# Kernel optimization log

Hardware: AMD Instinct MI355X
Metric: run time of the kernel (lower is better)

The kernel has to match this reference:

```python
import jax, jax.numpy as jnp
import numpy as np

B, DIM, N = 4, 256, 2048
DIM_CTX, M = 256, 2048
HEADS, DIM_HEAD = 8, 64
DIM_INNER = HEADS * DIM_HEAD  # 512
EPS = 1e-12  # matches F.normalize eps


def setup_inputs() -> dict:
    key = jax.random.key(0)
    ks = jax.random.split(key, 8)
    return {
        "fmap": jax.random.normal(ks[0], (B, DIM, N), dtype=jnp.float32),
        "context": jax.random.normal(ks[1], (B, DIM_CTX, M), dtype=jnp.float32),
        "mask": jax.random.randint(ks[2], (B, M), 0, 2) > 0,
        "gamma": jnp.ones((DIM, 1), dtype=jnp.float32),
        "gamma_ctx": jnp.ones((DIM_CTX, 1), dtype=jnp.float32),
        "Wq": jax.random.normal(ks[3], (DIM_INNER, DIM), dtype=jnp.float32) * (DIM ** -0.5),
        "Wkv": jax.random.normal(ks[4], (2 * DIM_INNER, DIM_CTX), dtype=jnp.float32) * (DIM_CTX ** -0.5),
        "Wout": jax.random.normal(ks[5], (DIM, DIM_INNER), dtype=jnp.float32) * (DIM_INNER ** -0.5),
    }


def channel_rmsnorm(x, gamma):
    # F.normalize(x, dim=1) * sqrt(dim) * gamma ; x: [b, c, n], gamma: [c, 1]
    scale = x.shape[1] ** 0.5
    norm = jnp.sqrt(jnp.sum(x * x, axis=1, keepdims=True))
    normed = x / jnp.maximum(norm, EPS)
    return normed * scale * gamma[None]


def reference(fmap, context, mask, gamma, gamma_ctx, Wq, Wkv, Wout):
    h, d = HEADS, DIM_HEAD
    attn_scale = d ** -0.5

    fmap_n = channel_rmsnorm(fmap, gamma)          # [b, dim, n]
    ctx_n = channel_rmsnorm(context, gamma_ctx)    # [b, dim_ctx, m]

    # 1x1 Conv1d == matmul over channels
    q = jnp.einsum('oc,bcn->bon', Wq, fmap_n)      # [b, h*d, n]
    kv = jnp.einsum('oc,bcm->bom', Wkv, ctx_n)     # [b, 2*h*d, m]
    k, v = jnp.split(kv, 2, axis=1)

    # [b, h*d, n] -> [b, h, n, d]
    def to_heads(t):
        b, _, nn = t.shape
        return t.reshape(b, h, d, nn).transpose(0, 1, 3, 2)

    q, k, v = to_heads(q), to_heads(k), to_heads(v)

    # L2-distance attention: sim = -||q_i - k_j||_2 * scale
    q2 = jnp.sum(q * q, axis=-1)                   # [b, h, n]
    k2 = jnp.sum(k * k, axis=-1)                   # [b, h, m]
    qk = jnp.einsum('bhid,bhjd->bhij', q, k)       # [b, h, n, m]
    d2 = jnp.maximum(q2[..., :, None] + k2[..., None, :] - 2.0 * qk, 0.0)
    dist = jnp.sqrt(jnp.maximum(d2, EPS))
    sim = -dist * attn_scale

    neg_max = -jnp.finfo(sim.dtype).max
    sim = jnp.where(mask[:, None, None, :], sim, neg_max)

    attn = jax.nn.softmax(sim, axis=-1)            # [b, h, n, m]
    out = jnp.einsum('bhij,bhjd->bhid', attn, v)   # [b, h, n, d]
    out = out.transpose(0, 1, 3, 2).reshape(out.shape[0], h * d, -1)  # [b, h*d, n]
    return jnp.einsum('oc,bcn->bon', Wout, out)    # [b, dim, n]
```

## Files before the change

### kernel.cpp

```cpp
#include <hip/hip_runtime.h>
#include <hip/hip_bf16.h>

#define B_ 4
#define DIM_ 256
#define N_ 2048
#define M_ 2048
#define HEADS_ 8
#define DHEAD_ 64
#define DINNER_ 512

typedef __attribute__((ext_vector_type(8))) short short8;
typedef __attribute__((ext_vector_type(4))) short short4v;
typedef __attribute__((ext_vector_type(4))) float floatx4;
typedef __attribute__((ext_vector_type(4))) _Float16 half4;
typedef __attribute__((ext_vector_type(8))) _Float16 half8;

#if defined(__has_builtin)
#if __has_builtin(__builtin_amdgcn_global_load_lds)
#define HAS_DMA 1
#endif
#endif

typedef __attribute__((address_space(1))) const void gvoid_t;
typedef __attribute__((address_space(3))) void lvoid_t;

#define CQ_ 0.18033688011112042f
#define NEG2CQ_ (-0.36067376022224084f)
#define EPS2_ 3.25213893e-14f

__device__ inline short bf16r(float x) {
  unsigned u = __float_as_uint(x);
  unsigned r = (u + 0x7fffu + ((u >> 16) & 1u)) >> 16;
  return (short)r;
}
__device__ inline float bf2f(short b) {
  return __uint_as_float(((unsigned)(unsigned short)b) << 16);
}

__global__ __launch_bounds__(256) void wsplit_kernel(
    const float* __restrict__ Wq, const float* __restrict__ Wkv,
    const float* __restrict__ Wout, const float* __restrict__ gamma,
    const float* __restrict__ gctx, short* __restrict__ whi,
    short* __restrict__ wlo) {
  const int y = blockIdx.y;
  const int gsz[3] = {32768, 65536, 32768};
  const int goff[3] = {0, 131072, 393216};
  int gidx = blockIdx.x * 256 + threadIdx.x;
  if (gidx >= gsz[y]) return;
  const float* W = (y == 0) ? Wq : (y == 1) ? Wkv : Wout;
  const int cmask = (y == 2) ? 511 : 255;
  int e0 = gidx * 4;
  int c = e0 & cmask;
  float4 wv = *(const float4*)&W[e0];
  if (y < 2) {
    const float* g = (y == 0) ? gamma : gctx;
    float4 g4 = *(const float4*)&g[c];
    wv.x *= g4.x; wv.y *= g4.y; wv.z *= g4.z; wv.w *= g4.w;
  }
  float vv[4] = {wv.x, wv.y, wv.z, wv.w};
  short4v hi, lo;
#pragma unroll
  for (int e = 0; e < 4; ++e) {
    short hb = bf16r(vv[e]);
    hi[e] = hb;
    lo[e] = bf16r(vv[e] - bf2f(hb));
  }
  *(short4v*)&whi[goff[y] + e0] = hi;
  *(short4v*)&wlo[goff[y] + e0] = lo;
}

__global__ __launch_bounds__(256) void colnorm_t_kernel(
    const float* __restrict__ xf, const float* __restrict__ xc,
    short* __restrict__ xtf, short* __restrict__ xtc, int NN) {
  const float* x = (blockIdx.z == 0) ? xf : xc;
  short* xt = (blockIdx.z == 0) ? xtf : xtc;
  int b = blockIdx.y;
  int tx = threadIdx.x, ty = threadIdx.y;
  int n0 = blockIdx.x * 64, n = n0 + tx;
  const float* xb = x + (size_t)b * 256 * NN;

  float ssq = 0.f;
  for (int c = ty; c < 256; c += 4) {
    float v = xb[(size_t)c * NN + n];
    ssq += v * v;
  }
  __shared__ float red[4][64];
  __shared__ float scl[64];
  __shared__ float t[64][65];
  red[ty][tx] = ssq;
  __syncthreads();
  if (ty == 0) {
    float s = red[0][tx] + red[1][tx] + red[2][tx] + red[3][tx];
    scl[tx] = 16.0f / fmaxf(sqrtf(s), 1e-12f);
  }
  int tid = ty * 64 + tx;
  int row = tid >> 2, cg = tid & 3;
  for (int c0 = 0; c0 < 256; c0 += 64) {
    __syncthreads();
    for (int cc = ty; cc < 64; cc += 4) t[cc][tx] = xb[(size_t)(c0 + cc) * NN + n];
    __syncthreads();
    float sc = scl[row];
    short8 o0v, o1v;
#pragma unroll
    for (int e = 0; e < 8; ++e) {
      o0v[e] = bf16r(t[cg * 16 + e][row] * sc);
      o1v[e] = bf16r(t[cg * 16 + 8 + e][row] * sc);
    }
    size_t base = ((size_t)b * NN + n0 + row) * 256 + c0 + cg * 16;
    *(short8*)&xt[base] = o0v;
    *(short8*)&xt[base + 8] = o1v;
  }
}

__global__ __launch_bounds__(256) void qkv_gemm_kernel(
    const short* __restrict__ whi, const short* __restrict__ wlo,
    const short* __restrict__ fmap_t, const short* __restrict__ ctx_t,
    short* __restrict__ qb, short* __restrict__ kc, _Float16* __restrict__ vc,
    const int* __restrict__ maskp, float* __restrict__ k2m) {
  const int b = blockIdx.z;
  const int y = blockIdx.y;
  const bool isq = (y < 4);
  const int o0 = (isq ? y : y - 4) * 128;
  const int n0 = blockIdx.x * 128;
  const short* Wh = whi + (isq ? 0 : 131072);
  const short* Wl = wlo + (isq ? 0 : 131072);
  const short* Xt = isq ? fmap_t : ctx_t;

  const int tid = threadIdx.x;
  const int w = tid >> 6, l = tid & 63, quad = l >> 4, l15 = l & 15;
  const int wo = (w >> 1) * 64, wn = (w & 1) * 64;

  __shared__ __align__(16) short Wa[2][128][40];
  __shared__ __align__(16) short Xb[128][40];

  floatx4 acc[4][4];
#pragma unroll
  for (int ot = 0; ot < 4; ++ot)
#pragma unroll
    for (int nt = 0; nt < 4; ++nt)
#pragma unroll
      for (int r = 0; r < 4; ++r) acc[ot][nt][r] = 0.f;

  for (int c0 = 0; c0 < 256; c0 += 32) {
    __syncthreads();
#pragma unroll
    for (int it = 0; it < 2; ++it) {
      int lin = tid + it * 256;
      int row = lin >> 2, sg = (lin & 3) * 8;
      size_t src = (size_t)(o0 + row) * 256 + c0 + sg;
      *(short8*)&Wa[0][row][sg] = *(const short8*)&Wh[src];
      *(short8*)&Wa[1][row][sg] = *(const short8*)&Wl[src];
    }
#pragma unroll
    for (int it = 0; it < 2; ++it) {
      int lin = tid + it * 256;
      int nn = lin >> 2, sg = (lin & 3) * 8;
      *(short8*)&Xb[nn][sg] =
          *(const short8*)&Xt[((size_t)b * 2048 + n0 + nn) * 256 + c0 + sg];
    }
    __syncthreads();

    short8 ah[4], al[4], bx[4];
#pragma unroll
    for (int ot = 0; ot < 4; ++ot) {
      ah[ot] = *(const short8*)&Wa[0][wo + 16 * ot + l15][8 * quad];
      al[ot] = *(const short8*)&Wa[1][wo + 16 * ot + l15][8 * quad];
    }
#pragma unroll
    for (int nt = 0; nt < 4; ++nt)
      bx[nt] = *(const short8*)&Xb[wn + 16 * nt + l15][8 * quad];
#pragma unroll
    for (int ot = 0; ot < 4; ++ot)
#pragma unroll
      for (int nt = 0; nt < 4; ++nt) {
        acc[ot][nt] =
            __builtin_amdgcn_mfma_f32_16x16x32_bf16(al[ot], bx[nt], acc[ot][nt], 0, 0, 0);
        acc[ot][nt] =
            __builtin_amdgcn_mfma_f32_16x16x32_bf16(ah[ot], bx[nt], acc[ot][nt], 0, 0, 0);
      }
  }

  if (isq) {
#pragma unroll
    for (int nt = 0; nt < 4; ++nt) {
      int n = n0 + wn + 16 * nt + l15;
      size_t base = ((size_t)b * 2048 + n) * 512;
#pragma unroll
      for (int ot = 0; ot < 4; ++ot) {
        int o = o0 + wo + 16 * ot + 4 * quad;
        short4v pk;
#pragma unroll
        for (int r = 0; r < 4; ++r) pk[r] = bf16r(CQ_ * acc[ot][nt][r]);
        *(short4v*)&qb[base + o] = pk;
      }
    }
  } else if (o0 < 512) {
    const int head = (o0 + wo) >> 6;
    const int bh = b * 8 + head;
    float k2p[4] = {0.f, 0.f, 0.f, 0.f};
#pragma unroll
    for (int nt = 0; nt < 4; ++nt) {
      int m = n0 + wn + 16 * nt + l15;
      int chunk = m >> 6, mrow = m & 63;
      size_t tbase = (((size_t)bh * 32 + chunk) * 64 + mrow) * 64;
      int sw = mrow & 7;
#pragma unroll
      for (int ot = 0; ot < 4; ++ot) {
        int d0 = 16 * ot + 4 * quad;
        short4v pk;
#pragma unroll
        for (int r = 0; r < 4; ++r) {
          short pv = bf16r(NEG2CQ_ * acc[ot][nt][r]);
          pk[r] = pv;
          float kr = bf2f(pv);
          k2p[nt] += kr * kr;
        }
        *(short4v*)&kc[tbase + (size_t)(((d0 >> 3) ^ sw) << 3) + (d0 & 7)] = pk;
      }
    }
#pragma unroll
    for (int nt = 0; nt < 4; ++nt) {
      float s = k2p[nt];
      s += __shfl_xor(s, 16);
      s += __shfl_xor(s, 32);
      if (quad == 0) {
        int m = n0 + wn + 16 * nt + l15;
        int mv = maskp[b * 2048 + m];
        k2m[(size_t)bh * 2048 + m] = mv ? 0.25f * s : __builtin_inff();
      }
    }
  } else {
    const int chv = o0 - 512 + wo;
    const int bh = b * 8 + (chv >> 6);
#pragma unroll
    for (int nt = 0; nt < 4; ++nt) {
      int j = n0 + wn + 16 * nt + l15;
      int chunk = j >> 6, jr = j & 63;
      int jrem = jr & 31;
      int colp = 32 * (jr >> 5) + ((jrem >> 2) & 3) * 8 + (jrem >> 4) * 4 +
                 (jrem & 3);
      size_t cbase = ((size_t)bh * 32 + chunk) * 4096;
#pragma unroll
      for (int ot = 0; ot < 4; ++ot)
#pragma unroll
        for (int r = 0; r < 4; ++r) {
          int drow = (chv + 16 * ot + 4 * quad + r) & 63;
          vc[cbase + drow * 64 + (((colp >> 3) ^ (drow & 7)) << 3) +
             (colp & 7)] = (_Float16)acc[ot][nt][r];
        }
    }
  }
}

__global__ __launch_bounds__(512, 8) void attn_kernel(
    const short* __restrict__ qb, const short* __restrict__ kc,
    const _Float16* __restrict__ vc, const float* __restrict__ k2m,
    short* __restrict__ attn_t) {
  const int bid = blockIdx.x;
  const int rr = bid & 7, qq = bid >> 3;
  const int bh = rr * 4 + (qq >> 5);
  const int iblk = qq & 31;
  const int h = bh & 7, b = bh >> 3;
  const int i0 = iblk * 64;

  const int tid = threadIdx.x;
  const int w = tid >> 6, l = tid & 63, quad = l >> 4, l15 = l & 15;
  const int wr = w >> 1, jh = w & 1;

  __shared__ __align__(16) short sbuf[2][2][4096];

  const short* qrow =
      qb + ((size_t)b * 2048 + i0 + 16 * wr + l15) * 512 + h * 64;
  const short* kcb = kc + (size_t)bh * 32 * 4096;
  const _Float16* vcb = vc + (size_t)bh * 32 * 4096;
  const float* k2b = k2m + (size_t)bh * 2048;

  short8 qa0 = *(const short8*)&qrow[8 * quad];
  short8 qa1 = *(const short8*)&qrow[32 + 8 * quad];
  float q2p = 0.f;
#pragma unroll
  for (int jj = 0; jj < 8; ++jj) {
    float f0 = bf2f(qa0[jj]), f1 = bf2f(qa1[jj]);
    q2p += f0 * f0 + f1 * f1;
  }
  q2p += __shfl_xor(q2p, 16);
  q2p += __shfl_xor(q2p, 32);
  const float q2c = q2p;

  floatx4 accO[4];
#pragma unroll
  for (int dt = 0; dt < 4; ++dt)
#pragma unroll
    for (int r = 0; r < 4; ++r) accO[dt][r] = 0.f;
  float lsum = 0.f;

  const int sx = l15 & 7;

  auto stage = [&](int c, int p) {
    const short* ks = kcb + (size_t)c * 4096 + w * 512 + l * 8;
    const _Float16* vs = vcb + (size_t)c * 4096 + w * 512 + l * 8;
#ifdef HAS_DMA
    __builtin_amdgcn_global_load_lds((gvoid_t*)ks,
                                     (lvoid_t*)&sbuf[0][p][w * 512], 16, 0, 0);
    __builtin_amdgcn_global_load_lds((gvoid_t*)vs,
                                     (lvoid_t*)&sbuf[1][p][w * 512], 16, 0, 0);
#else
    *(short8*)&sbuf[0][p][w * 512 + l * 8] = *(const short8*)ks;
    *(half8*)&((_Float16*)sbuf[1][p])[w * 512 + l * 8] = *(const half8*)vs;
#endif
  };

  stage(0, 0);
  for (int c = 0; c < 32; ++c) {
    __syncthreads();
    if (c < 31) stage(c + 1, (c + 1) & 1);
    const int p = c & 1;

    half8 pb;
#pragma unroll
    for (int jt = 0; jt < 2; ++jt) {
      float4 k2v = *(const float4*)&k2b[c * 64 + jh * 32 + 16 * jt + 4 * quad];
      const short* kr = &sbuf[0][p][(jh * 32 + 16 * jt + l15) * 64];
      short8 k0 = *(const short8*)&kr[(quad ^ sx) << 3];
      short8 k1 = *(const short8*)&kr[((quad + 4) ^ sx) << 3];
      floatx4 a;
      a[0] = q2c + k2v.x;
      a[1] = q2c + k2v.y;
      a[2] = q2c + k2v.z;
      a[3] = q2c + k2v.w;
      __builtin_amdgcn_s_setprio(1);
      a = __builtin_amdgcn_mfma_f32_16x16x32_bf16(k0, qa0, a, 0, 0, 0);
      a = __builtin_amdgcn_mfma_f32_16x16x32_bf16(k1, qa1, a, 0, 0, 0);
      __builtin_amdgcn_s_setprio(0);
#pragma unroll
      for (int r = 0; r < 4; ++r) {
        float s = __builtin_amdgcn_sqrtf(fmaxf(a[r], EPS2_));
        float pv = __builtin_amdgcn_exp2f(-s);
        lsum += pv;
        pb[4 * jt + r] = (_Float16)pv;
      }
    }

    __builtin_amdgcn_s_setprio(1);
#pragma unroll
    for (int dt = 0; dt < 4; ++dt) {
      const _Float16* vr = (const _Float16*)&sbuf[1][p][(16 * dt + l15) * 64];
      half8 hh = *(const half8*)&vr[((quad + 4 * jh) ^ sx) << 3];
      accO[dt] =
          __builtin_amdgcn_mfma_f32_16x16x32_f16(hh, pb, accO[dt], 0, 0, 0);
    }
    __builtin_amdgcn_s_setprio(0);
  }

  __syncthreads();
  float* scr = (float*)sbuf;
  const int sidx = (wr * 64 + l) * 17;
  if (jh) {
#pragma unroll
    for (int dt = 0; dt < 4; ++dt)
#pragma unroll
      for (int r = 0; r < 4; ++r) scr[sidx + dt * 4 + r] = accO[dt][r];
    scr[sidx + 16] = lsum;
  }
  __syncthreads();
  if (!jh) {
#pragma unroll
    for (int dt = 0; dt < 4; ++dt)
#pragma unroll
      for (int r = 0; r < 4; ++r) accO[dt][r] += scr[sidx + dt * 4 + r];
    lsum += scr[sidx + 16];
    lsum += __shfl_xor(lsum, 16);
    lsum += __shfl_xor(lsum, 32);
    float rl = 1.0f / lsum;
    size_t base = ((size_t)b * 2048 + i0 + 16 * wr + l15) * 512 + h * 64;
#pragma unroll
    for (int dt = 0; dt < 4; ++dt) {
      short4v pk;
#pragma unroll
      for (int r = 0; r < 4; ++r) pk[r] = bf16r(accO[dt][r] * rl);
      *(short4v*)&attn_t[base + 16 * dt + 4 * quad] = pk;
    }
  }
}

__global__ __launch_bounds__(256) void outproj_kernel(
    const short* __restrict__ whi, const short* __restrict__ wlo,
    const short* __restrict__ Xt, float* __restrict__ Yf) {
  const int b = blockIdx.z;
  const int n0 = blockIdx.x * 128;
  const int o0 = blockIdx.y * 64;
  const int tid = threadIdx.x;
  const int w = tid >> 6, l = tid & 63, quad = l >> 4, l15 = l & 15;
  const int wo = (w >> 1) * 32, wn = (w & 1) * 64;

  __shared__ __align__(16) short Wa[2][64][40];
  __shared__ __align__(16) short Xb[128][40];

  floatx4 acc[2][4];
#pragma unroll
  for (int ot = 0; ot < 2; ++ot)
#pragma unroll
    for (int nt = 0; nt < 4; ++nt)
#pragma unroll
      for (int r = 0; r < 4; ++r) acc[ot][nt][r] = 0.f;

  for (int c0 = 0; c0 < 512; c0 += 32) {
    __syncthreads();
    {
      int row = tid >> 2, sg = (tid & 3) * 8;
      size_t src = (size_t)(o0 + row) * 512 + c0 + sg;
      *(short8*)&Wa[0][row][sg] = *(const short8*)&whi[src];
      *(short8*)&Wa[1][row][sg] = *(const short8*)&wlo[src];
    }
#pragma unroll
    for (int it = 0; it < 2; ++it) {
      int lin = tid + it * 256;
      int nn = lin >> 2, sg = (lin & 3) * 8;
      *(short8*)&Xb[nn][sg] =
          *(const short8*)&Xt[((size_t)b * 2048 + n0 + nn) * 512 + c0 + sg];
    }
    __syncthreads();

    short8 ah[2], al[2], bx[4];
#pragma unroll
    for (int ot = 0; ot < 2; ++ot) {
      ah[ot] = *(const short8*)&Wa[0][wo + 16 * ot + l15][8 * quad];
      al[ot] = *(const short8*)&Wa[1][wo + 16 * ot + l15][8 * quad];
    }
#pragma unroll
    for (int nt = 0; nt < 4; ++nt)
      bx[nt] = *(const short8*)&Xb[wn + 16 * nt + l15][8 * quad];
#pragma unroll
    for (int ot = 0; ot < 2; ++ot)
#pragma unroll
      for (int nt = 0; nt < 4; ++nt) {
        acc[ot][nt] =
            __builtin_amdgcn_mfma_f32_16x16x32_bf16(al[ot], bx[nt], acc[ot][nt], 0, 0, 0);
        acc[ot][nt] =
            __builtin_amdgcn_mfma_f32_16x16x32_bf16(ah[ot], bx[nt], acc[ot][nt], 0, 0, 0);
      }
  }

#pragma unroll
  for (int ot = 0; ot < 2; ++ot)
#pragma unroll
    for (int r = 0; r < 4; ++r) {
      int o = o0 + wo + 16 * ot + 4 * quad + r;
#pragma unroll
      for (int nt = 0; nt < 4; ++nt)
        Yf[((size_t)b * 256 + o) * 2048 + n0 + wn + 16 * nt + l15] =
            acc[ot][nt][r];
    }
}

extern "C" void kernel_launch(void* const* d_in, const int* in_sizes, int n_in,
                              void* d_out, int out_size, void* d_ws,
                              size_t ws_size, hipStream_t stream) {
  const float* fmap = (const float*)d_in[0];
  const float* context = (const float*)d_in[1];
  const int* mask = (const int*)d_in[2];
  const float* gamma = (const float*)d_in[3];
  const float* gamma_ctx = (const float*)d_in[4];
  const float* Wq = (const float*)d_in[5];
  const float* Wkv = (const float*)d_in[6];
  const float* Wout = (const float*)d_in[7];
  float* out = (float*)d_out;

  char* ws = (char*)d_ws;
  short* fmap_t = (short*)ws;
  short* ctx_t = fmap_t + 2097152;
  short* qb = ctx_t + 2097152;
  short* kc = qb + 4194304;
  _Float16* vc = (_Float16*)(kc + 4194304);
  short* attn_t = (short*)(vc + 4194304);
  float* k2m = (float*)(attn_t + 4194304);
  short* whi = (short*)(k2m + 65536);
  short* wlo = whi + 524288;

  dim3 blk64x4(64, 4);
  wsplit_kernel<<<dim3(256, 3), 256, 0, stream>>>(Wq, Wkv, Wout, gamma,
                                                  gamma_ctx, whi, wlo);
  colnorm_t_kernel<<<dim3(32, B_, 2), blk64x4, 0, stream>>>(
      fmap, context, fmap_t, ctx_t, N_);
  qkv_gemm_kernel<<<dim3(16, 12, B_), 256, 0, stream>>>(
      whi, wlo, fmap_t, ctx_t, qb, kc, vc, mask, k2m);
  attn_kernel<<<dim3(1024), 512, 0, stream>>>(qb, kc, vc, k2m, attn_t);
  outproj_kernel<<<dim3(16, 4, B_), 256, 0, stream>>>(whi + 393216,
                                                      wlo + 393216, attn_t,
                                                      out);
}
```

Measured before the change: 206.3 us.

## Software-pipeline PV MFMA one chunk behind QK and softmax in attention loop

Restructures the attention main loop so the P·V MFMAs for chunk c-1 are issued while chunk c's QK MFMAs and sqrt/exp2 work are in flight. V staging is delayed by one iteration into its own double buffer, and K gets its own double buffer. A final epilogue applies the last chunk's PV. The aim is to overlap transcendental VALU work with matrix-core work and remove the serial dependency between softmax and PV within an iteration. In exchange, the probabilities must stay live across iterations, which adds register pressure, and V is loaded with less lead time before it is used.

```diff
diff --git a/kernel.cpp b/kernel.cpp
--- a/kernel.cpp
+++ b/kernel.cpp
@@ -267,7 +267,7 @@
   const int w = tid >> 6, l = tid & 63, quad = l >> 4, l15 = l & 15;
   const int wr = w >> 1, jh = w & 1;
 
-  __shared__ __align__(16) short sbuf[2][2][4096];
+  __shared__ __align__(16) short sbuf[4][4096];
 
   const short* qrow =
       qb + ((size_t)b * 2048 + i0 + 16 * wr + l15) * 512 + h * 64;
@@ -296,60 +296,97 @@
 
   const int sx = l15 & 7;
 
-  auto stage = [&](int c, int p) {
+  auto stageK = [&](int c, int p) {
     const short* ks = kcb + (size_t)c * 4096 + w * 512 + l * 8;
+#ifdef HAS_DMA
+    __builtin_amdgcn_global_load_lds((gvoid_t*)ks,
+                                     (lvoid_t*)&sbuf[p][w * 512], 16, 0, 0);
+#else
+    *(short8*)&sbuf[p][w * 512 + l * 8] = *(const short8*)ks;
+#endif
+  };
+  auto stageV = [&](int c, int p) {
     const _Float16* vs = vcb + (size_t)c * 4096 + w * 512 + l * 8;
 #ifdef HAS_DMA
-    __builtin_amdgcn_global_load_lds((gvoid_t*)ks,
-                                     (lvoid_t*)&sbuf[0][p][w * 512], 16, 0, 0);
     __builtin_amdgcn_global_load_lds((gvoid_t*)vs,
-                                     (lvoid_t*)&sbuf[1][p][w * 512], 16, 0, 0);
+                                     (lvoid_t*)&sbuf[2 + p][w * 512], 16, 0, 0);
 #else
-    *(short8*)&sbuf[0][p][w * 512 + l * 8] = *(const short8*)ks;
-    *(half8*)&((_Float16*)sbuf[1][p])[w * 512 + l * 8] = *(const half8*)vs;
+    *(half8*)&((_Float16*)sbuf[2 + p])[w * 512 + l * 8] = *(const half8*)vs;
 #endif
   };
 
-  stage(0, 0);
+  stageK(0, 0);
+  half8 pbprev;
   for (int c = 0; c < 32; ++c) {
     __syncthreads();
-    if (c < 31) stage(c + 1, (c + 1) & 1);
     const int p = c & 1;
-
-    half8 pb;
-#pragma unroll
-    for (int jt = 0; jt < 2; ++jt) {
-      float4 k2v = *(const float4*)&k2b[c * 64 + jh * 32 + 16 * jt + 4 * quad];
-      const short* kr = &sbuf[0][p][(jh * 32 + 16 * jt + l15) * 64];
+    if (c < 31) stageK(c + 1, p ^ 1);
+    stageV(c, p);
+
+    floatx4 a0, a1;
+    {
+      float4 k2v = *(const float4*)&k2b[c * 64 + jh * 32 + 4 * quad];
+      const short* kr = &sbuf[p][(jh * 32 + l15) * 64];
       short8 k0 = *(const short8*)&kr[(quad ^ sx) << 3];
       short8 k1 = *(const short8*)&kr[((quad + 4) ^ sx) << 3];
-      floatx4 a;
-      a[0] = q2c + k2v.x;
-      a[1] = q2c + k2v.y;
-      a[2] = q2c + k2v.z;
-      a[3] = q2c + k2v.w;
+      a0[0] = q2c + k2v.x; a0[1] = q2c + k2v.y;
+      a0[2] = q2c + k2v.z; a0[3] = q2c + k2v.w;
       __builtin_amdgcn_s_setprio(1);
-      a = __builtin_amdgcn_mfma_f32_16x16x32_bf16(k0, qa0, a, 0, 0, 0);
-      a = __builtin_amdgcn_mfma_f32_16x16x32_bf16(k1, qa1, a, 0, 0, 0);
+      a0 = __builtin_amdgcn_mfma_f32_16x16x32_bf16(k0, qa0, a0, 0, 0, 0);
+      a0 = __builtin_amdgcn_mfma_f32_16x16x32_bf16(k1, qa1, a0, 0, 0, 0);
       __builtin_amdgcn_s_setprio(0);
-#pragma unroll
-      for (int r = 0; r < 4; ++r) {
-        float s = __builtin_amdgcn_sqrtf(fmaxf(a[r], EPS2_));
-        float pv = __builtin_amdgcn_exp2f(-s);
-        lsum += pv;
-        pb[4 * jt + r] = (_Float16)pv;
+    }
+    {
+      float4 k2v = *(const float4*)&k2b[c * 64 + jh * 32 + 16 + 4 * quad];
+      const short* kr = &sbuf[p][(jh * 32 + 16 + l15) * 64];
+      short8 k0 = *(const short8*)&kr[(quad ^ sx) << 3];
+      short8 k1 = *(const short8*)&kr[((quad + 4) ^ sx) << 3];
+      a1[0] = q2c + k2v.x; a1[1] = q2c + k2v.y;
+      a1[2] = q2c + k2v.z; a1[3] = q2c + k2v.w;
+      __builtin_amdgcn_s_setprio(1);
+      a1 = __builtin_amdgcn_mfma_f32_16x16x32_bf16(k0, qa0, a1, 0, 0, 0);
+      a1 = __builtin_amdgcn_mfma_f32_16x16x32_bf16(k1, qa1, a1, 0, 0, 0);
+      __builtin_amdgcn_s_setprio(0);
+    }
+
+    if (c > 0) {
+      __builtin_amdgcn_s_setprio(1);
+#pragma unroll
+      for (int dt = 0; dt < 4; ++dt) {
+        const _Float16* vr =
+            (const _Float16*)&sbuf[2 + (p ^ 1)][(16 * dt + l15) * 64];
+        half8 hh = *(const half8*)&vr[((quad + 4 * jh) ^ sx) << 3];
+        accO[dt] =
+            __builtin_amdgcn_mfma_f32_16x16x32_f16(hh, pbprev, accO[dt], 0, 0, 0);
       }
-    }
-
-    __builtin_amdgcn_s_setprio(1);
-#pragma unroll
-    for (int dt = 0; dt < 4; ++dt) {
-      const _Float16* vr = (const _Float16*)&sbuf[1][p][(16 * dt + l15) * 64];
-      half8 hh = *(const half8*)&vr[((quad + 4 * jh) ^ sx) << 3];
-      accO[dt] =
-          __builtin_amdgcn_mfma_f32_16x16x32_f16(hh, pb, accO[dt], 0, 0, 0);
-    }
-    __builtin_amdgcn_s_setprio(0);
+      __builtin_amdgcn_s_setprio(0);
+    }
+
+    half8 pb;
+#pragma unroll
+    for (int r = 0; r < 4; ++r) {
+      float s = __builtin_amdgcn_sqrtf(fmaxf(a0[r], EPS2_));
+      float pv = __builtin_amdgcn_exp2f(-s);
+      lsum += pv;
+      pb[r] = (_Float16)pv;
+    }
+#pragma unroll
+    for (int r = 0; r < 4; ++r) {
+      float s = __builtin_amdgcn_sqrtf(fmaxf(a1[r], EPS2_));
+      float pv = __builtin_amdgcn_exp2f(-s);
+      lsum += pv;
+      pb[4 + r] = (_Float16)pv;
+    }
+    pbprev = pb;
+  }
+
+  __syncthreads();
+#pragma unroll
+  for (int dt = 0; dt < 4; ++dt) {
+    const _Float16* vr = (const _Float16*)&sbuf[3][(16 * dt + l15) * 64];
+    half8 hh = *(const half8*)&vr[((quad + 4 * jh) ^ sx) << 3];
+    accO[dt] =
+        __builtin_amdgcn_mfma_f32_16x16x32_f16(hh, pbprev, accO[dt], 0, 0, 0);
   }
 
   __syncthreads();
```

Measured after the change: 211.5 us. 2.6% more time.
